# Kernel optimization log

Measured on AMD Instinct MI355X. Metric: run time of the kernel, lower is better.

Reference implementation:

```python
import jax, jax.numpy as jnp
import numpy as np

E, N, G = 102400, 100000, 64
D_NODE, D_EDGE, D_GLOB, K = 256, 256, 128, 4
LAYERS = [512, 512, 256]
LN_EPS = 1e-3  # keras LayerNormalization default epsilon


def setup_inputs() -> dict:
    key = jax.random.key(0)
    ks = jax.random.split(key, 12)
    d_in = D_EDGE + K * D_NODE + D_GLOB  # 1408
    inp = {
        "feat": jax.random.normal(ks[0], (E, D_EDGE), jnp.float32),
        "nodes": jax.random.normal(ks[1], (N, D_NODE), jnp.float32),
        "gfeat": jax.random.normal(ks[2], (G, D_GLOB), jnp.float32),
        "ind": jax.random.randint(ks[3], (E, K), 0, N, jnp.int32),
        "num": jnp.full((G,), E // G, jnp.int32),  # sum(num) == E
    }
    dims = [d_in] + LAYERS
    for i in range(3):
        scale = 1.0 / np.sqrt(dims[i])
        inp[f"W{i+1}"] = jax.random.normal(ks[4 + i], (dims[i], dims[i + 1]), jnp.float32) * scale
        inp[f"b{i+1}"] = jnp.zeros((dims[i + 1],), jnp.float32)
    inp["gamma"] = jnp.ones((LAYERS[-1],), jnp.float32)
    inp["beta"] = jnp.zeros((LAYERS[-1],), jnp.float32)
    return inp


def reference(feat, nodes, gfeat, ind, num, W1, b1, W2, b2, W3, b3, gamma, beta):
    e = feat.shape[0]
    # _fixed_number_to_one: gather K nodes per hyperedge, flatten -> [E, K*D_NODE]
    gathered = nodes[ind].reshape(e, -1)
    # _one_to_segments: broadcast per-graph globals to their edges -> [E, D_GLOB]
    graph_ids = jnp.repeat(jnp.arange(num.shape[0]), num, total_repeat_length=e)
    glob = gfeat[graph_ids]
    x = jnp.concatenate([feat, gathered, glob], axis=1)  # [E, 1408]
    h = jax.nn.relu(x @ W1 + b1)
    h = jax.nn.relu(h @ W2 + b2)
    h = jax.nn.sigmoid(h @ W3 + b3)
    # keras LayerNormalization over the last axis
    mu = jnp.mean(h, axis=-1, keepdims=True)
    var = jnp.var(h, axis=-1, keepdims=True)
    return gamma * (h - mu) * jax.lax.rsqrt(var + LN_EPS) + beta
```

## Files before the change

### kernel.cpp

```cpp
#include <hip/hip_runtime.h>
#include <hip/hip_fp16.h>

#define E_EDGES 102400
#define N_NODES 100000
#define G_GRAPHS 64
#define D_EDGE 256
#define D_NODE 256
#define D_GLOB 128
#define KNB 4
#define D_IN 1408
#define H1D 512
#define H2D 512
#define H3D 256
#define LN_EPS 1e-3f

typedef _Float16 half8 __attribute__((ext_vector_type(8)));
typedef float f32x4 __attribute__((ext_vector_type(4)));

__device__ __forceinline__ void gload16(const void* g, void* l) {
    __builtin_amdgcn_global_load_lds((const __attribute__((address_space(1))) void*)g,
                                     (__attribute__((address_space(3))) void*)l, 16, 0, 0);
}


__global__ void k_prefix(const int* __restrict__ num, int* __restrict__ prefix) {
    if (threadIdx.x == 0) {
        int acc = 0;
        prefix[0] = 0;
        for (int g = 0; g < G_GRAPHS; ++g) { acc += num[g]; prefix[g + 1] = acc; }
    }
}

__global__ void k_gid(const int* __restrict__ prefix, int* __restrict__ gid) {
    int e = blockIdx.x * blockDim.x + threadIdx.x;
    if (e >= E_EDGES) return;
    int lo = 0, hi = G_GRAPHS;
    while (hi - lo > 1) {
        int mid = (lo + hi) >> 1;
        if (e >= prefix[mid]) lo = mid; else hi = mid;
    }
    gid[e] = lo;
}

__global__ void k_transpose(const float* __restrict__ src, _Float16* __restrict__ dst,
                            int Ks, int Ns) {
    long total = (long)Ks * Ns;
    for (long idx = (long)blockIdx.x * blockDim.x + threadIdx.x; idx < total;
         idx += (long)gridDim.x * blockDim.x) {
        int n = (int)(idx / Ks);
        int k = (int)(idx - (long)n * Ks);
        dst[idx] = (_Float16)src[(long)k * Ns + n];
    }
}

__global__ void k_cvt16(const float* __restrict__ src, _Float16* __restrict__ dst, long n8) {
    for (long i = (long)blockIdx.x * blockDim.x + threadIdx.x; i < n8;
         i += (long)gridDim.x * blockDim.x) {
        float4 u = reinterpret_cast<const float4*>(src)[i * 2];
        float4 v = reinterpret_cast<const float4*>(src)[i * 2 + 1];
        half8 h;
        h[0] = (_Float16)u.x; h[1] = (_Float16)u.y; h[2] = (_Float16)u.z; h[3] = (_Float16)u.w;
        h[4] = (_Float16)v.x; h[5] = (_Float16)v.y; h[6] = (_Float16)v.z; h[7] = (_Float16)v.w;
        reinterpret_cast<half8*>(dst)[i] = h;
    }
}


template <int KD, bool GATHER>
__global__ __launch_bounds__(512) void k_gemm_pipe(
    const _Float16* __restrict__ A,
    const _Float16* __restrict__ feat16, const _Float16* __restrict__ nodes16,
    const _Float16* __restrict__ gfeat16,
    const int* __restrict__ ind, const int* __restrict__ gid,
    const _Float16* __restrict__ Wt,
    const float* __restrict__ bias, _Float16* __restrict__ out) {
    constexpr int NT = KD / 64;
    __shared__ __align__(16) char lds[3 * 49152];

    const int t = threadIdx.x;
    const int bn = blockIdx.x, bm = blockIdx.y;
    const int n0 = bn * 256;
    const int w = t >> 6, lane = t & 63;
    const int wr = w >> 2, wc = w & 3;
    const int lr = lane & 15, lk = lane >> 4;

    const int srow = t >> 3;
    const int gslot = (t & 7) ^ (srow & 7);
    const int wbase = w * 8;

    int4 iv0, iv1;
    int g0 = 0, g1 = 0;
    int e0 = 0, e1 = 0;
    if constexpr (GATHER) {
        e0 = bm * 128 + srow;
        e1 = e0 + 64;
        iv0 = *reinterpret_cast<const int4*>(ind + (size_t)e0 * KNB);
        iv1 = *reinterpret_cast<const int4*>(ind + (size_t)e1 * KNB);
        g0 = gid[e0];
        g1 = gid[e1];
    }

    f32x4 acc[4][4];
#pragma unroll
    for (int m = 0; m < 4; m++)
#pragma unroll
        for (int n = 0; n < 4; n++) acc[m][n] = (f32x4)0.f;

    auto stage = [&](int kt, char* abuf, char* bbuf) {
#pragma unroll
        for (int c = 0; c < 2; ++c) {
            const _Float16* src;
            if constexpr (GATHER) {
                if (kt < 4) {
                    src = feat16 + (size_t)(c ? e1 : e0) * D_EDGE + kt * 64;
                } else if (kt < 20) {
                    int j = (kt - 4) >> 2;
                    int4 iv = c ? iv1 : iv0;
                    int nidx = j == 0 ? iv.x : j == 1 ? iv.y : j == 2 ? iv.z : iv.w;
                    src = nodes16 + (size_t)nidx * D_NODE + ((kt - 4) & 3) * 64;
                } else {
                    src = gfeat16 + (size_t)(c ? g1 : g0) * D_GLOB + (kt - 20) * 64;
                }
            } else {
                src = A + (size_t)(bm * 128 + c * 64 + srow) * KD + kt * 64;
            }
            gload16(src + gslot * 8, abuf + (c * 64 + wbase) * 128);
        }
#pragma unroll
        for (int c = 0; c < 4; ++c) {
            const _Float16* src = Wt + (size_t)(n0 + c * 64 + srow) * KD + kt * 64;
            gload16(src + gslot * 8, bbuf + (c * 64 + wbase) * 128);
        }
    };

    stage(0, lds, lds + 16384);
    stage(1, lds + 49152, lds + 49152 + 16384);
    asm volatile("s_waitcnt vmcnt(6)" ::: "memory");
    __builtin_amdgcn_s_barrier();

    int cur = 0;
    for (int kt = 0; kt < NT; ++kt) {
        const int pf = kt + 2;
        if (pf < NT) {
            const int pb = cur == 0 ? 2 : cur - 1;
            stage(pf, lds + pb * 49152, lds + pb * 49152 + 16384);
        }
        const char* ab = lds + cur * 49152;
        const char* bb = ab + 16384;
#pragma unroll
        for (int kk = 0; kk < 2; ++kk) {
            half8 a[4], b[4];
#pragma unroll
            for (int m = 0; m < 4; ++m) {
                int row = wr * 64 + m * 16 + lr;
                a[m] = *reinterpret_cast<const half8*>(
                    ab + row * 128 + ((((kk << 2) | lk)) ^ (lr & 7)) * 16);
            }
#pragma unroll
            for (int n = 0; n < 4; ++n) {
                int row = wc * 64 + n * 16 + lr;
                b[n] = *reinterpret_cast<const half8*>(
                    bb + row * 128 + ((((kk << 2) | lk)) ^ (lr & 7)) * 16);
            }
            __builtin_amdgcn_s_setprio(1);
#pragma unroll
            for (int m = 0; m < 4; ++m)
#pragma unroll
                for (int n = 0; n < 4; ++n)
                    acc[m][n] = __builtin_amdgcn_mfma_f32_16x16x32_f16(a[m], b[n], acc[m][n], 0, 0, 0);
            __builtin_amdgcn_s_setprio(0);
        }
        if (pf < NT) asm volatile("s_waitcnt vmcnt(6)" ::: "memory");
        else         asm volatile("s_waitcnt vmcnt(0)" ::: "memory");
        __builtin_amdgcn_s_barrier();
        cur = cur == 2 ? 0 : cur + 1;
    }

#pragma unroll
    for (int n = 0; n < 4; ++n) {
        int col = n0 + wc * 64 + n * 16 + lr;
        float bv = bias[col];
#pragma unroll
        for (int m = 0; m < 4; ++m) {
            int rbase = bm * 128 + wr * 64 + m * 16 + lk * 4;
#pragma unroll
            for (int q = 0; q < 4; ++q) {
                float v = acc[m][n][q] + bv;
                v = v > 0.f ? v : 0.f;
                out[(size_t)(rbase + q) * H1D + col] = (_Float16)v;
            }
        }
    }
}


__global__ __launch_bounds__(512) void k_gemm3_ln(
    const _Float16* __restrict__ A, const _Float16* __restrict__ Wt,
    const float* __restrict__ bias, const float* __restrict__ gamma,
    const float* __restrict__ beta, float* __restrict__ out) {
    __shared__ __align__(16) _Float16 As[128][64];
    __shared__ __align__(16) _Float16 Bs[256][64];
    __shared__ float red1[128][4];
    __shared__ float red2[128][4];
    __shared__ float mvmu[128];
    __shared__ float mvrs[128];
    const int t = threadIdx.x;
    const int bm = blockIdx.x;
    const int w = t >> 6, lane = t & 63;
    const int wr = w >> 2, wc = w & 3, lr = lane & 15, lk = lane >> 4;

    const int srow = w * 8 + (lane >> 3);
    const int scol = (lane & 7) * 8;
    const _Float16* Ab = A + (size_t)(bm * 128 + srow) * H2D + scol;
    const _Float16* Bb = Wt + (size_t)srow * H2D + scol;

    f32x4 acc[4][4];
#pragma unroll
    for (int m = 0; m < 4; m++)
#pragma unroll
        for (int n = 0; n < 4; n++) acc[m][n] = (f32x4)0.f;

    for (int kt = 0; kt < 8; ++kt) {
        const int k0 = kt * 64;
        __syncthreads();
#pragma unroll
        for (int i = 0; i < 2; i++)
            gload16(Ab + (size_t)i * 64 * H2D + k0, (char*)As + i * 8192 + w * 1024);
#pragma unroll
        for (int i = 0; i < 4; i++)
            gload16(Bb + (size_t)i * 64 * H2D + k0, (char*)Bs + i * 8192 + w * 1024);
        __syncthreads();
#pragma unroll
        for (int kk = 0; kk < 2; kk++) {
            half8 a[4], b[4];
#pragma unroll
            for (int m = 0; m < 4; m++)
                a[m] = *reinterpret_cast<half8*>(&As[wr * 64 + m * 16 + lr][kk * 32 + lk * 8]);
#pragma unroll
            for (int n = 0; n < 4; n++)
                b[n] = *reinterpret_cast<half8*>(&Bs[wc * 64 + n * 16 + lr][kk * 32 + lk * 8]);
#pragma unroll
            for (int m = 0; m < 4; m++)
#pragma unroll
                for (int n = 0; n < 4; n++)
                    acc[m][n] = __builtin_amdgcn_mfma_f32_16x16x32_f16(a[m], b[n], acc[m][n], 0, 0, 0);
        }
    }

#pragma unroll
    for (int n = 0; n < 4; n++) {
        int col = wc * 64 + n * 16 + lr;
        float bv = bias[col];
#pragma unroll
        for (int m = 0; m < 4; m++)
#pragma unroll
            for (int q = 0; q < 4; q++) {
                float x = acc[m][n][q] + bv;
                acc[m][n][q] = 1.f / (1.f + __expf(-x));
            }
    }

#pragma unroll
    for (int m = 0; m < 4; m++)
#pragma unroll
        for (int q = 0; q < 4; q++) {
            float s1 = 0.f, s2 = 0.f;
#pragma unroll
            for (int n = 0; n < 4; n++) {
                float x = acc[m][n][q];
                s1 += x; s2 += x * x;
            }
            s1 += __shfl_xor(s1, 1); s2 += __shfl_xor(s2, 1);
            s1 += __shfl_xor(s1, 2); s2 += __shfl_xor(s2, 2);
            s1 += __shfl_xor(s1, 4); s2 += __shfl_xor(s2, 4);
            s1 += __shfl_xor(s1, 8); s2 += __shfl_xor(s2, 8);
            if (lr == 0) {
                int row = wr * 64 + m * 16 + lk * 4 + q;
                red1[row][wc] = s1;
                red2[row][wc] = s2;
            }
        }
    __syncthreads();
    if (t < 128) {
        float s = red1[t][0] + red1[t][1] + red1[t][2] + red1[t][3];
        float ss = red2[t][0] + red2[t][1] + red2[t][2] + red2[t][3];
        float mu = s * (1.f / H3D);
        float var = ss * (1.f / H3D) - mu * mu;
        mvmu[t] = mu;
        mvrs[t] = rsqrtf(var + LN_EPS);
    }
    __syncthreads();
#pragma unroll
    for (int m = 0; m < 4; m++)
#pragma unroll
        for (int q = 0; q < 4; q++) {
            int row = wr * 64 + m * 16 + lk * 4 + q;
            float mu = mvmu[row], rs = mvrs[row];
#pragma unroll
            for (int n = 0; n < 4; n++) {
                int col = wc * 64 + n * 16 + lr;
                out[(size_t)(bm * 128 + row) * H3D + col] =
                    gamma[col] * (acc[m][n][q] - mu) * rs + beta[col];
            }
        }
}


extern "C" void kernel_launch(void* const* d_in, const int* in_sizes, int n_in,
                              void* d_out, int out_size, void* d_ws, size_t ws_size,
                              hipStream_t stream) {
    const float* feat  = (const float*)d_in[0];
    const float* nodes = (const float*)d_in[1];
    const float* gfeat = (const float*)d_in[2];
    const int*   ind   = (const int*)d_in[3];
    const int*   num   = (const int*)d_in[4];
    const float* W1    = (const float*)d_in[5];
    const float* b1    = (const float*)d_in[6];
    const float* W2    = (const float*)d_in[7];
    const float* b2    = (const float*)d_in[8];
    const float* W3    = (const float*)d_in[9];
    const float* b3    = (const float*)d_in[10];
    const float* gamma = (const float*)d_in[11];
    const float* beta  = (const float*)d_in[12];
    float* out = (float*)d_out;

    char* ws = (char*)d_ws;
    size_t off = 0;
    auto alloc = [&](size_t bytes) {
        size_t o = off;
        off += (bytes + 255) & ~(size_t)255;
        return o;
    };
    int* prefix       = (int*)(ws + alloc((G_GRAPHS + 1) * sizeof(int)));
    int* gid          = (int*)(ws + alloc((size_t)E_EDGES * sizeof(int)));
    _Float16* W1t     = (_Float16*)(ws + alloc((size_t)H1D * D_IN * 2));
    _Float16* W2t     = (_Float16*)(ws + alloc((size_t)H2D * H1D * 2));
    _Float16* W3t     = (_Float16*)(ws + alloc((size_t)H3D * H2D * 2));
    _Float16* feat16  = (_Float16*)(ws + alloc((size_t)E_EDGES * D_EDGE * 2));
    _Float16* nodes16 = (_Float16*)(ws + alloc((size_t)N_NODES * D_NODE * 2));
    _Float16* gfeat16 = (_Float16*)(ws + alloc((size_t)G_GRAPHS * D_GLOB * 2));
    _Float16* h1      = (_Float16*)(ws + alloc((size_t)E_EDGES * H1D * 2));
    _Float16* h2      = (_Float16*)(ws + alloc((size_t)E_EDGES * H2D * 2));
    (void)ws_size; (void)in_sizes; (void)n_in; (void)out_size;

    k_prefix<<<1, 64, 0, stream>>>(num, prefix);
    k_gid<<<(E_EDGES + 255) / 256, 256, 0, stream>>>(prefix, gid);
    k_cvt16<<<2048, 256, 0, stream>>>(feat, feat16, (long)E_EDGES * D_EDGE / 8);
    k_cvt16<<<2048, 256, 0, stream>>>(nodes, nodes16, (long)N_NODES * D_NODE / 8);
    k_cvt16<<<16, 256, 0, stream>>>(gfeat, gfeat16, (long)G_GRAPHS * D_GLOB / 8);
    k_transpose<<<1024, 256, 0, stream>>>(W1, W1t, D_IN, H1D);
    k_transpose<<<512, 256, 0, stream>>>(W2, W2t, H1D, H2D);
    k_transpose<<<256, 256, 0, stream>>>(W3, W3t, H2D, H3D);
    k_gemm_pipe<D_IN, true><<<dim3(H1D / 256, E_EDGES / 128), 512, 0, stream>>>(
        nullptr, feat16, nodes16, gfeat16, ind, gid, W1t, b1, h1);
    k_gemm_pipe<H1D, false><<<dim3(H2D / 256, E_EDGES / 128), 512, 0, stream>>>(
        h1, nullptr, nullptr, nullptr, nullptr, nullptr, W2t, b2, h2);
    k_gemm3_ln<<<E_EDGES / 128, 512, 0, stream>>>(h2, W3t, b3, gamma, beta, out);
}
```

Baseline: 629.9 us.

## Enlarge GEMM tiles to 256x256 with double-buffered phased prefetch

The first two MLP GEMMs now use 256x256 output tiles per block instead of 128x256, with each wave computing 128x64. The three-stage LDS ring is replaced by a 128KB double buffer, and next-tile loads are interleaved across four compute phases separated by barriers. This raises arithmetic intensity per staged byte and halves the block count. In exchange it doubles accumulator register pressure (launch_bounds 512,2 may force spills) and adds more barriers per k-step.

```diff
diff --git a/kernel.cpp b/kernel.cpp
--- a/kernel.cpp
+++ b/kernel.cpp
@@ -67,7 +67,7 @@
 
 
 template <int KD, bool GATHER>
-__global__ __launch_bounds__(512) void k_gemm_pipe(
+__global__ __launch_bounds__(512, 2) void k_gemm8(
     const _Float16* __restrict__ A,
     const _Float16* __restrict__ feat16, const _Float16* __restrict__ nodes16,
     const _Float16* __restrict__ gfeat16,
@@ -75,7 +75,7 @@
     const _Float16* __restrict__ Wt,
     const float* __restrict__ bias, _Float16* __restrict__ out) {
     constexpr int NT = KD / 64;
-    __shared__ __align__(16) char lds[3 * 49152];
+    __shared__ __align__(16) char lds[131072];
 
     const int t = threadIdx.x;
     const int bn = blockIdx.x, bm = blockIdx.y;
@@ -86,94 +86,115 @@
 
     const int srow = t >> 3;
     const int gslot = (t & 7) ^ (srow & 7);
-    const int wbase = w * 8;
-
-    int4 iv0, iv1;
-    int g0 = 0, g1 = 0;
-    int e0 = 0, e1 = 0;
+    const int ldst = w * 1024;
+
+    int e0 = 0, e1 = 0, e2 = 0, e3 = 0, g0 = 0, g1 = 0, g2 = 0, g3 = 0;
+    int4 v0, v1, v2, v3;
     if constexpr (GATHER) {
-        e0 = bm * 128 + srow;
-        e1 = e0 + 64;
-        iv0 = *reinterpret_cast<const int4*>(ind + (size_t)e0 * KNB);
-        iv1 = *reinterpret_cast<const int4*>(ind + (size_t)e1 * KNB);
-        g0 = gid[e0];
-        g1 = gid[e1];
-    }
-
-    f32x4 acc[4][4];
-#pragma unroll
-    for (int m = 0; m < 4; m++)
+        e0 = bm * 256 + srow; e1 = e0 + 64; e2 = e0 + 128; e3 = e0 + 192;
+        v0 = *reinterpret_cast<const int4*>(ind + (size_t)e0 * KNB);
+        v1 = *reinterpret_cast<const int4*>(ind + (size_t)e1 * KNB);
+        v2 = *reinterpret_cast<const int4*>(ind + (size_t)e2 * KNB);
+        v3 = *reinterpret_cast<const int4*>(ind + (size_t)e3 * KNB);
+        g0 = gid[e0]; g1 = gid[e1]; g2 = gid[e2]; g3 = gid[e3];
+    }
+
+    auto stageA = [&](int kt, int u, char* db) {
+        const _Float16* s;
+        if constexpr (GATHER) {
+            const int e = (u == 0 ? e0 : u == 1 ? e1 : u == 2 ? e2 : e3);
+            if (kt < 4) {
+                s = feat16 + (size_t)e * D_EDGE + kt * 64;
+            } else if (kt < 20) {
+                const int4 iv = (u == 0 ? v0 : u == 1 ? v1 : u == 2 ? v2 : v3);
+                int j = (kt - 4) >> 2;
+                int nid = j == 0 ? iv.x : j == 1 ? iv.y : j == 2 ? iv.z : iv.w;
+                s = nodes16 + (size_t)nid * D_NODE + ((kt - 4) & 3) * 64;
+            } else {
+                const int g = (u == 0 ? g0 : u == 1 ? g1 : u == 2 ? g2 : g3);
+                s = gfeat16 + (size_t)g * D_GLOB + (kt - 20) * 64;
+            }
+        } else {
+            s = A + (size_t)(bm * 256 + u * 64 + srow) * KD + kt * 64;
+        }
+        gload16(s + gslot * 8, db + u * 8192 + ldst);
+    };
+    auto stageB = [&](int kt, int u, char* db) {
+        const _Float16* s = Wt + (size_t)(n0 + u * 64 + srow) * KD + kt * 64;
+        gload16(s + gslot * 8, db + 32768 + u * 8192 + ldst);
+    };
+
+    f32x4 acc[8][4];
+#pragma unroll
+    for (int m = 0; m < 8; m++)
 #pragma unroll
         for (int n = 0; n < 4; n++) acc[m][n] = (f32x4)0.f;
 
-    auto stage = [&](int kt, char* abuf, char* bbuf) {
-#pragma unroll
-        for (int c = 0; c < 2; ++c) {
-            const _Float16* src;
-            if constexpr (GATHER) {
-                if (kt < 4) {
-                    src = feat16 + (size_t)(c ? e1 : e0) * D_EDGE + kt * 64;
-                } else if (kt < 20) {
-                    int j = (kt - 4) >> 2;
-                    int4 iv = c ? iv1 : iv0;
-                    int nidx = j == 0 ? iv.x : j == 1 ? iv.y : j == 2 ? iv.z : iv.w;
-                    src = nodes16 + (size_t)nidx * D_NODE + ((kt - 4) & 3) * 64;
-                } else {
-                    src = gfeat16 + (size_t)(c ? g1 : g0) * D_GLOB + (kt - 20) * 64;
-                }
-            } else {
-                src = A + (size_t)(bm * 128 + c * 64 + srow) * KD + kt * 64;
-            }
-            gload16(src + gslot * 8, abuf + (c * 64 + wbase) * 128);
-        }
-#pragma unroll
-        for (int c = 0; c < 4; ++c) {
-            const _Float16* src = Wt + (size_t)(n0 + c * 64 + srow) * KD + kt * 64;
-            gload16(src + gslot * 8, bbuf + (c * 64 + wbase) * 128);
-        }
-    };
-
-    stage(0, lds, lds + 16384);
-    stage(1, lds + 49152, lds + 49152 + 16384);
+    char* d0 = lds;
+    char* d1 = lds + 65536;
+
+    stageB(0, 0, d0); stageB(0, 1, d0); stageB(0, 2, d0); stageB(0, 3, d0);
+    stageA(0, 0, d0); stageA(0, 1, d0); stageA(0, 2, d0); stageA(0, 3, d0);
+    if (NT > 1) {
+        stageB(1, 0, d1); stageB(1, 1, d1); stageB(1, 2, d1); stageB(1, 3, d1);
+        stageA(1, 1, d1); stageA(1, 3, d1);
+    }
     asm volatile("s_waitcnt vmcnt(6)" ::: "memory");
     __builtin_amdgcn_s_barrier();
 
-    int cur = 0;
     for (int kt = 0; kt < NT; ++kt) {
-        const int pf = kt + 2;
-        if (pf < NT) {
-            const int pb = cur == 0 ? 2 : cur - 1;
-            stage(pf, lds + pb * 49152, lds + pb * 49152 + 16384);
-        }
-        const char* ab = lds + cur * 49152;
-        const char* bb = ab + 16384;
-#pragma unroll
-        for (int kk = 0; kk < 2; ++kk) {
-            half8 a[4], b[4];
-#pragma unroll
-            for (int m = 0; m < 4; ++m) {
-                int row = wr * 64 + m * 16 + lr;
-                a[m] = *reinterpret_cast<const half8*>(
-                    ab + row * 128 + ((((kk << 2) | lk)) ^ (lr & 7)) * 16);
-            }
-#pragma unroll
-            for (int n = 0; n < 4; ++n) {
-                int row = wc * 64 + n * 16 + lr;
-                b[n] = *reinterpret_cast<const half8*>(
-                    bb + row * 128 + ((((kk << 2) | lk)) ^ (lr & 7)) * 16);
+        char* db = lds + (kt & 1) * 65536;
+        char* odb = lds + ((kt + 1) & 1) * 65536;
+        half8 bfr[4][2];
+#pragma unroll
+        for (int p = 0; p < 4; ++p) {
+            const int mb = 6 - 2 * p;
+            half8 afr[2][2];
+#pragma unroll
+            for (int mm = 0; mm < 2; ++mm) {
+                int row = wr * 128 + (mb + mm) * 16 + lr;
+                int u = row >> 6, r = row & 63;
+#pragma unroll
+                for (int kk = 0; kk < 2; ++kk)
+                    afr[mm][kk] = *reinterpret_cast<const half8*>(
+                        db + u * 8192 + r * 128 + ((((kk << 2) | lk)) ^ (r & 7)) * 16);
+            }
+            if (p == 0) {
+#pragma unroll
+                for (int n = 0; n < 4; ++n) {
+                    int r = (wc * 64 + n * 16 + lr) & 63;
+#pragma unroll
+                    for (int kk = 0; kk < 2; ++kk)
+                        bfr[n][kk] = *reinterpret_cast<const half8*>(
+                            db + 32768 + wc * 8192 + r * 128 + ((((kk << 2) | lk)) ^ (r & 7)) * 16);
+                }
+            }
+            __builtin_amdgcn_s_barrier();
+            if (p == 0) {
+                if (kt + 1 < NT) { stageA(kt + 1, 0, odb); stageA(kt + 1, 2, odb); }
+            } else if (p == 1) {
+                if (kt + 2 < NT) { stageB(kt + 2, 0, db); stageB(kt + 2, 1, db); }
+            } else if (p == 2) {
+                if (kt + 2 < NT) { stageB(kt + 2, 2, db); stageB(kt + 2, 3, db); }
+            } else {
+                if (kt + 2 < NT) { stageA(kt + 2, 1, db); stageA(kt + 2, 3, db); }
             }
             __builtin_amdgcn_s_setprio(1);
 #pragma unroll
-            for (int m = 0; m < 4; ++m)
+            for (int mm = 0; mm < 2; ++mm)
 #pragma unroll
                 for (int n = 0; n < 4; ++n)
-                    acc[m][n] = __builtin_amdgcn_mfma_f32_16x16x32_f16(a[m], b[n], acc[m][n], 0, 0, 0);
+#pragma unroll
+                    for (int kk = 0; kk < 2; ++kk)
+                        acc[mb + mm][n] = __builtin_amdgcn_mfma_f32_16x16x32_f16(
+                            afr[mm][kk], bfr[n][kk], acc[mb + mm][n], 0, 0, 0);
             __builtin_amdgcn_s_setprio(0);
-        }
-        if (pf < NT) asm volatile("s_waitcnt vmcnt(6)" ::: "memory");
-        else         asm volatile("s_waitcnt vmcnt(0)" ::: "memory");
-        __builtin_amdgcn_s_barrier();
-        cur = cur == 2 ? 0 : cur + 1;
+            if (p == 3) {
+                if (kt + 2 < NT) asm volatile("s_waitcnt vmcnt(6)" ::: "memory");
+                else             asm volatile("s_waitcnt vmcnt(0)" ::: "memory");
+            }
+            __builtin_amdgcn_s_barrier();
+        }
     }
 
 #pragma unroll
@@ -181,8 +202,8 @@
         int col = n0 + wc * 64 + n * 16 + lr;
         float bv = bias[col];
 #pragma unroll
-        for (int m = 0; m < 4; ++m) {
-            int rbase = bm * 128 + wr * 64 + m * 16 + lk * 4;
+        for (int m = 0; m < 8; ++m) {
+            int rbase = bm * 256 + wr * 128 + m * 16 + lk * 4;
 #pragma unroll
             for (int q = 0; q < 4; ++q) {
                 float v = acc[m][n][q] + bv;
@@ -351,9 +372,9 @@
     k_transpose<<<1024, 256, 0, stream>>>(W1, W1t, D_IN, H1D);
     k_transpose<<<512, 256, 0, stream>>>(W2, W2t, H1D, H2D);
     k_transpose<<<256, 256, 0, stream>>>(W3, W3t, H2D, H3D);
-    k_gemm_pipe<D_IN, true><<<dim3(H1D / 256, E_EDGES / 128), 512, 0, stream>>>(
+    k_gemm8<D_IN, true><<<dim3(H1D / 256, E_EDGES / 256), 512, 0, stream>>>(
         nullptr, feat16, nodes16, gfeat16, ind, gid, W1t, b1, h1);
-    k_gemm_pipe<H1D, false><<<dim3(H2D / 256, E_EDGES / 128), 512, 0, stream>>>(
+    k_gemm8<H1D, false><<<dim3(H2D / 256, E_EDGES / 256), 512, 0, stream>>>(
         h1, nullptr, nullptr, nullptr, nullptr, nullptr, W2t, b2, h2);
     k_gemm3_ln<<<E_EDGES / 128, 512, 0, stream>>>(h2, W3t, b3, gamma, beta, out);
 }
```

Result: slower. 649.2 us (+3.1%).
